# Kernel optimization log

Measured on AMD Instinct MI355X. Metric: run time of the kernel, lower is better.

## Reference

```python
import jax, jax.numpy as jnp
import numpy as np

# dims matching init_kwargs
B, C, T = 64, 8, 2048
K, DIL = 16, 4            # kernel_size, dilation
MLP = 16                  # mlp_dim
NF = min(MLP, K // 2 + 1) # n_frequencies = 9
FEAT = C * NF * 2         # 144
H1, H2 = 64, 32           # ReLUBlock hidden dims (64 -> 64//2)
EFF = DIL * (K - 1)       # 60
W = T - EFF               # 1988 windows


def setup_inputs() -> dict:
    key = jax.random.key(0)
    ks = jax.random.split(key, 10)
    def lin(k, out_d, in_d):
        kw, kb = jax.random.split(k)
        bound = 1.0 / np.sqrt(in_d)
        w = jax.random.uniform(kw, (out_d, in_d), jnp.float32, -bound, bound)
        b = jax.random.uniform(kb, (out_d,), jnp.float32, -bound, bound)
        return w, b
    x = jax.random.normal(ks[0], (B, C, T), jnp.float32)
    proj_w, proj_b = lin(ks[1], MLP, FEAT)
    w1, b1 = lin(ks[2], H1, MLP)
    w2, b2 = lin(ks[3], H2, H1)
    out_w, out_b = lin(ks[4], 1, H2)
    agg_w = jax.random.normal(ks[5], (W,), jnp.float32) * 0.1
    return {"x": x, "proj_w": proj_w, "proj_b": proj_b, "w1": w1, "b1": b1,
            "w2": w2, "b2": b2, "out_w": out_w, "out_b": out_b, "agg_w": agg_w}


def reference(x, proj_w, proj_b, w1, b1, w2, b2, out_w, out_b, agg_w):
    # Build all dilated windows at once: window[t, j] = x[..., t - (K-1-j)*DIL]
    starts = jnp.arange(EFF, T)                      # [W]
    offs = -(K - 1 - jnp.arange(K)) * DIL            # [K]
    idx = starts[:, None] + offs[None, :]            # [W, K]
    win = x[:, :, idx]                               # [B, C, W, K]
    f = jnp.fft.rfft(win, axis=-1)[..., :NF]         # [B, C, W, NF]
    mag = jnp.log1p(jnp.abs(f))
    ph = jnp.angle(f) / jnp.pi
    feat = jnp.stack([mag, ph], axis=-1)             # [B, C, W, NF, 2]
    feat = feat.transpose(0, 2, 1, 3, 4).reshape(B, W, FEAT)  # [B, W, C*NF*2]
    p = jnp.tanh(feat @ proj_w.T + proj_b) * jnp.pi  # [B, W, MLP]
    h = jax.nn.relu(p @ w1.T + b1)                   # [B, W, H1]
    h = jax.nn.relu(h @ w2.T + b2)                   # [B, W, H2]
    out = (h @ out_w.T + out_b)[..., 0]              # [B, W]
    wts = jax.nn.softmax(agg_w)                      # [W]
    return (out * wts[None, :]).sum(axis=1)          # [B]
```

## Files before the change

kernel.cpp:

```cpp
#include <hip/hip_runtime.h>
#include <math.h>

#define B_    64
#define C_    8
#define T_    2048
#define K_    16
#define NF_   9
#define FEAT_ 144
#define MLP_  16
#define H1_   64
#define H2_   32
#define EFF_  60
#define W_    1988
#define NWCH_ 8
#define PI_F  3.14159265358979323846f

constexpr float COS16[16] = {
   1.0f,  0.92387953251128674f,  0.70710678118654752f,  0.38268343236508977f,
   0.0f, -0.38268343236508977f, -0.70710678118654752f, -0.92387953251128674f,
  -1.0f, -0.92387953251128674f, -0.70710678118654752f, -0.38268343236508977f,
   0.0f,  0.38268343236508977f,  0.70710678118654752f,  0.92387953251128674f };
constexpr float SIN16[16] = {
   0.0f,  0.38268343236508977f,  0.70710678118654752f,  0.92387953251128674f,
   1.0f,  0.92387953251128674f,  0.70710678118654752f,  0.38268343236508977f,
   0.0f, -0.38268343236508977f, -0.70710678118654752f, -0.92387953251128674f,
   0.0f, -0.92387953251128674f, -0.70710678118654752f, -0.38268343236508977f };
constexpr float SIN16F[16] = {
   0.0f,  0.38268343236508977f,  0.70710678118654752f,  0.92387953251128674f,
   1.0f,  0.92387953251128674f,  0.70710678118654752f,  0.38268343236508977f,
   0.0f, -0.38268343236508977f, -0.70710678118654752f, -0.92387953251128674f,
  -1.0f, -0.92387953251128674f, -0.70710678118654752f, -0.38268343236508977f };

__device__ __forceinline__ float fast_log1p(float s) {
  return __builtin_amdgcn_logf(1.0f + s) * 0.69314718055994531f;
}

__device__ __forceinline__ float atanpi_poly(float r) {
  const float s2 = r * r;
  float p = -0.0037310f;
  p = fmaf(p, s2,  0.0167600f);
  p = fmaf(p, s2, -0.0370617f);
  p = fmaf(p, s2,  0.0616068f);
  p = fmaf(p, s2, -0.10587734f);
  p = fmaf(p, s2,  0.31830265f);
  return r * p;
}

__device__ __forceinline__ float atan2pi_fast(float im, float re) {
  const float ax = fabsf(re), ay = fabsf(im);
  const float mx = fmaxf(ax, ay), mn = fminf(ax, ay);
  const float r = mn * __builtin_amdgcn_rcpf(fmaxf(mx, 1e-37f));
  float t = atanpi_poly(r);
  t = (ay > ax) ? 0.5f - t : t;
  t = (__float_as_uint(re) & 0x80000000u) ? 1.0f - t : t;
  return copysignf(t, im);
}

__device__ __forceinline__ float fast_tanh(float z) {
  const float az = fabsf(z);
  const float e = __builtin_amdgcn_exp2f(-2.8853900817779268f * az);
  const float th = fmaf(-2.0f, e * __builtin_amdgcn_rcpf(1.0f + e), 1.0f);
  return copysignf(th, z);
}

__global__ __launch_bounds__(256) void prep_kernel(const float* __restrict__ pw,
                                                   const float* __restrict__ w2,
                                                   float* __restrict__ PWt,
                                                   float* __restrict__ W2t) {
  const int tid = blockIdx.x * 256 + threadIdx.x;
  if (tid < MLP_ * FEAT_) {
    const int j = tid / FEAT_, f = tid - j * FEAT_;
    PWt[f * MLP_ + j] = pw[tid];
  }
  if (tid < H2_ * H1_) {
    const int m = tid >> 6, i = tid & 63;
    W2t[i * H2_ + m] = w2[tid];
  }
}

__global__ __launch_bounds__(256) void softmax_kernel(const float* __restrict__ agg,
                                                      float* __restrict__ wts) {
  __shared__ float red[256];
  const int tid = threadIdx.x;
  float m = -INFINITY;
  for (int i = tid; i < W_; i += 256) m = fmaxf(m, agg[i]);
  red[tid] = m; __syncthreads();
  for (int s = 128; s > 0; s >>= 1) { if (tid < s) red[tid] = fmaxf(red[tid], red[tid+s]); __syncthreads(); }
  const float mx = red[0];
  __syncthreads();
  float sum = 0.f;
  for (int i = tid; i < W_; i += 256) sum += expf(agg[i] - mx);
  red[tid] = sum; __syncthreads();
  for (int s = 128; s > 0; s >>= 1) { if (tid < s) red[tid] += red[tid+s]; __syncthreads(); }
  const float inv = 1.f / red[0];
  for (int i = tid; i < W_; i += 256) wts[i] = expf(agg[i] - mx) * inv;
}

__global__ __launch_bounds__(256) void tcn_main(
    const float* __restrict__ x,
    const float* __restrict__ PWt, const float* __restrict__ proj_b,
    const float* __restrict__ w1, const float* __restrict__ b1,
    const float* __restrict__ W2t, const float* __restrict__ b2,
    const float* __restrict__ out_w, const float* __restrict__ out_b,
    const float* __restrict__ wts, float* __restrict__ partials) {
  __shared__ float red[256];
  const int tid = threadIdx.x;
  const int b = blockIdx.y;
  const int w = blockIdx.x * 256 + tid;
  float val = 0.f;
  if (w < W_) {
    float pacc[MLP_];
    #pragma unroll
    for (int j = 0; j < MLP_; j++) pacc[j] = proj_b[j];

    const float* xb = x + (size_t)(b * C_) * T_ + w;
    #pragma unroll 1
    for (int c = 0; c < C_; c++) {
      const float* xc = xb + c * T_;
      float win[K_];
      #pragma unroll
      for (int k = 0; k < K_; k++) win[k] = xc[k * 4];

      float ae[8], bo[8];
      #pragma unroll
      for (int k = 0; k < 8; k++) { ae[k] = win[k] + win[k+8]; bo[k] = win[k] - win[k+8]; }

      #pragma unroll
      for (int n = 0; n < NF_; n++) {
        float re = 0.f, im = 0.f;
        #pragma unroll
        for (int k = 0; k < 8; k++) {
          const float v = (n & 1) ? bo[k] : ae[k];
          const int t = (n * k) & 15;
          re = fmaf(v,  COS16[t],  re);
          im = fmaf(v, -SIN16F[t], im);
        }
        const float m2  = fmaf(re, re, im * im);
        const float s   = __builtin_amdgcn_sqrtf(m2);
        const float mag = fast_log1p(s);
        const float ph  = atan2pi_fast(im, re);

        const float* rm = PWt + (size_t)((c * NF_ + n) * 2) * MLP_;
        #pragma unroll
        for (int j = 0; j < MLP_; j++)
          pacc[j] = fmaf(mag, rm[j], fmaf(ph, rm[MLP_ + j], pacc[j]));
      }
    }

    float p[MLP_];
    #pragma unroll
    for (int j = 0; j < MLP_; j++) p[j] = fast_tanh(pacc[j]) * PI_F;

    float h2a[H2_];
    #pragma unroll
    for (int m = 0; m < H2_; m++) h2a[m] = b2[m];

    #pragma unroll 8
    for (int i = 0; i < H1_; i++) {
      const float* r1 = w1 + i * MLP_;
      float acc = b1[i];
      #pragma unroll
      for (int j = 0; j < MLP_; j++) acc = fmaf(p[j], r1[j], acc);
      const float h1v = fmaxf(acc, 0.f);
      const float* r2 = W2t + i * H2_;
      #pragma unroll
      for (int m = 0; m < H2_; m++) h2a[m] = fmaf(h1v, r2[m], h2a[m]);
    }

    float o = out_b[0];
    #pragma unroll
    for (int m = 0; m < H2_; m++) o = fmaf(fmaxf(h2a[m], 0.f), out_w[m], o);
    val = o * wts[w];
  }

  red[tid] = val; __syncthreads();
  for (int s = 128; s > 0; s >>= 1) { if (tid < s) red[tid] += red[tid+s]; __syncthreads(); }
  if (tid == 0) partials[b * gridDim.x + blockIdx.x] = red[0];
}

__global__ void finalize_kernel(const float* __restrict__ partials, float* __restrict__ out) {
  const int b = threadIdx.x;
  if (b < B_) {
    float s = 0.f;
    #pragma unroll
    for (int c = 0; c < NWCH_; c++) s += partials[b * NWCH_ + c];
    out[b] = s;
  }
}

extern "C" void kernel_launch(void* const* d_in, const int* in_sizes, int n_in,
                              void* d_out, int out_size, void* d_ws, size_t ws_size,
                              hipStream_t stream) {
  const float* x      = (const float*)d_in[0];
  const float* proj_w = (const float*)d_in[1];
  const float* proj_b = (const float*)d_in[2];
  const float* w1     = (const float*)d_in[3];
  const float* b1     = (const float*)d_in[4];
  const float* w2     = (const float*)d_in[5];
  const float* b2     = (const float*)d_in[6];
  const float* out_w  = (const float*)d_in[7];
  const float* out_b  = (const float*)d_in[8];
  const float* agg_w  = (const float*)d_in[9];

  float* wts      = (float*)d_ws;
  float* partials = (float*)d_ws + 2048;
  float* PWt      = (float*)d_ws + 4096;
  float* W2t      = (float*)d_ws + 4096 + 2304;

  prep_kernel<<<9, 256, 0, stream>>>(proj_w, w2, PWt, W2t);
  softmax_kernel<<<1, 256, 0, stream>>>(agg_w, wts);
  tcn_main<<<dim3(NWCH_, B_), 256, 0, stream>>>(x, PWt, proj_b, w1, b1, W2t, b2,
                                                out_w, out_b, wts, partials);
  finalize_kernel<<<1, 64, 0, stream>>>(partials, (float*)d_out);
}
```

Measured before the change: 60.71 us.

## Split each window across four waves over channels and hidden units

Each block now handles 64 windows instead of 256. Its four waves split the per-window work: each wave computes the DFT features for two channels and 16 of the 64 first-hidden units. Partial projection sums and partial second-layer sums are combined through shared memory, and the final reduction uses wave shuffles. The grid grows from 512 to 2048 blocks so more waves can run on the GPU at once. In exchange it adds several block barriers and shared-memory traffic, and the finalize kernel sums 32 partials per batch row.

```diff
diff --git a/kernel.cpp b/kernel.cpp
--- a/kernel.cpp
+++ b/kernel.cpp
@@ -12,7 +12,7 @@
 #define H2_   32
 #define EFF_  60
 #define W_    1988
-#define NWCH_ 8
+#define NCHK_ 32
 #define PI_F  3.14159265358979323846f
 
 constexpr float COS16[16] = {
@@ -20,11 +20,6 @@
    0.0f, -0.38268343236508977f, -0.70710678118654752f, -0.92387953251128674f,
   -1.0f, -0.92387953251128674f, -0.70710678118654752f, -0.38268343236508977f,
    0.0f,  0.38268343236508977f,  0.70710678118654752f,  0.92387953251128674f };
-constexpr float SIN16[16] = {
-   0.0f,  0.38268343236508977f,  0.70710678118654752f,  0.92387953251128674f,
-   1.0f,  0.92387953251128674f,  0.70710678118654752f,  0.38268343236508977f,
-   0.0f, -0.38268343236508977f, -0.70710678118654752f, -0.92387953251128674f,
-   0.0f, -0.92387953251128674f, -0.70710678118654752f, -0.38268343236508977f };
 constexpr float SIN16F[16] = {
    0.0f,  0.38268343236508977f,  0.70710678118654752f,  0.92387953251128674f,
    1.0f,  0.92387953251128674f,  0.70710678118654752f,  0.38268343236508977f,
@@ -103,79 +98,110 @@
     const float* __restrict__ W2t, const float* __restrict__ b2,
     const float* __restrict__ out_w, const float* __restrict__ out_b,
     const float* __restrict__ wts, float* __restrict__ partials) {
-  __shared__ float red[256];
-  const int tid = threadIdx.x;
-  const int b = blockIdx.y;
-  const int w = blockIdx.x * 256 + tid;
-  float val = 0.f;
-  if (w < W_) {
-    float pacc[MLP_];
-    #pragma unroll
-    for (int j = 0; j < MLP_; j++) pacc[j] = proj_b[j];
-
-    const float* xb = x + (size_t)(b * C_) * T_ + w;
-    #pragma unroll 1
-    for (int c = 0; c < C_; c++) {
-      const float* xc = xb + c * T_;
-      float win[K_];
+  __shared__ float buf[4096];
+  const int tid  = threadIdx.x;
+  const int lane = tid & 63;
+  const int cg   = tid >> 6;
+  const int b     = blockIdx.y;
+  const int chunk = blockIdx.x;
+  const int w  = chunk * 64 + lane;
+  const int wl = (w < W_) ? w : (W_ - 1);
+
+  float pacc[MLP_];
+  #pragma unroll
+  for (int j = 0; j < MLP_; j++) pacc[j] = 0.f;
+
+  #pragma unroll
+  for (int cc = 0; cc < 2; cc++) {
+    const int c = cg + cc * 4;
+    const float* xc = x + ((size_t)b * C_ + c) * T_ + wl;
+    float win[K_];
+    #pragma unroll
+    for (int k = 0; k < K_; k++) win[k] = xc[k * 4];
+
+    float ae[8], bo[8];
+    #pragma unroll
+    for (int k = 0; k < 8; k++) { ae[k] = win[k] + win[k+8]; bo[k] = win[k] - win[k+8]; }
+
+    #pragma unroll
+    for (int n = 0; n < NF_; n++) {
+      float re = 0.f, im = 0.f;
       #pragma unroll
-      for (int k = 0; k < K_; k++) win[k] = xc[k * 4];
-
-      float ae[8], bo[8];
+      for (int k = 0; k < 8; k++) {
+        const float v = (n & 1) ? bo[k] : ae[k];
+        const int t = (n * k) & 15;
+        re = fmaf(v,  COS16[t],  re);
+        im = fmaf(v, -SIN16F[t], im);
+      }
+      const float s   = __builtin_amdgcn_sqrtf(fmaf(re, re, im * im));
+      const float mag = fast_log1p(s);
+      const float ph  = atan2pi_fast(im, re);
+      const float* rm = PWt + (size_t)((c * NF_ + n) * 2) * MLP_;
       #pragma unroll
-      for (int k = 0; k < 8; k++) { ae[k] = win[k] + win[k+8]; bo[k] = win[k] - win[k+8]; }
-
-      #pragma unroll
-      for (int n = 0; n < NF_; n++) {
-        float re = 0.f, im = 0.f;
-        #pragma unroll
-        for (int k = 0; k < 8; k++) {
-          const float v = (n & 1) ? bo[k] : ae[k];
-          const int t = (n * k) & 15;
-          re = fmaf(v,  COS16[t],  re);
-          im = fmaf(v, -SIN16F[t], im);
-        }
-        const float m2  = fmaf(re, re, im * im);
-        const float s   = __builtin_amdgcn_sqrtf(m2);
-        const float mag = fast_log1p(s);
-        const float ph  = atan2pi_fast(im, re);
-
-        const float* rm = PWt + (size_t)((c * NF_ + n) * 2) * MLP_;
-        #pragma unroll
-        for (int j = 0; j < MLP_; j++)
-          pacc[j] = fmaf(mag, rm[j], fmaf(ph, rm[MLP_ + j], pacc[j]));
-      }
+      for (int j = 0; j < MLP_; j++)
+        pacc[j] = fmaf(mag, rm[j], fmaf(ph, rm[MLP_ + j], pacc[j]));
     }
-
-    float p[MLP_];
-    #pragma unroll
-    for (int j = 0; j < MLP_; j++) p[j] = fast_tanh(pacc[j]) * PI_F;
-
-    float h2a[H2_];
-    #pragma unroll
-    for (int m = 0; m < H2_; m++) h2a[m] = b2[m];
-
-    #pragma unroll 8
-    for (int i = 0; i < H1_; i++) {
-      const float* r1 = w1 + i * MLP_;
-      float acc = b1[i];
-      #pragma unroll
-      for (int j = 0; j < MLP_; j++) acc = fmaf(p[j], r1[j], acc);
-      const float h1v = fmaxf(acc, 0.f);
-      const float* r2 = W2t + i * H2_;
-      #pragma unroll
-      for (int m = 0; m < H2_; m++) h2a[m] = fmaf(h1v, r2[m], h2a[m]);
+  }
+
+  #pragma unroll
+  for (int j = 0; j < MLP_; j++) buf[(j * 4 + cg) * 64 + lane] = pacc[j];
+  __syncthreads();
+
+  float p[MLP_];
+  #pragma unroll
+  for (int j = 0; j < MLP_; j++) {
+    const float* r = &buf[j * 256];
+    const float s01 = r[lane] + r[64 + lane];
+    const float s23 = r[128 + lane] + r[192 + lane];
+    p[j] = fast_tanh(s01 + s23 + proj_b[j]) * PI_F;
+  }
+  __syncthreads();
+
+  float h2a[H2_];
+  #pragma unroll
+  for (int m = 0; m < H2_; m++) h2a[m] = 0.f;
+
+  #pragma unroll 4
+  for (int ii = 0; ii < 16; ii++) {
+    const int i = cg * 16 + ii;
+    const float* r1 = w1 + i * MLP_;
+    float acc = b1[i];
+    #pragma unroll
+    for (int j = 0; j < MLP_; j++) acc = fmaf(p[j], r1[j], acc);
+    const float h1v = fmaxf(acc, 0.f);
+    const float* r2 = W2t + i * H2_;
+    #pragma unroll
+    for (int m = 0; m < H2_; m++) h2a[m] = fmaf(h1v, r2[m], h2a[m]);
+  }
+
+  if (cg >= 2) {
+    #pragma unroll
+    for (int m = 0; m < H2_; m++) buf[(m * 2 + (cg - 2)) * 64 + lane] = h2a[m];
+  }
+  __syncthreads();
+  if (cg < 2) {
+    #pragma unroll
+    for (int m = 0; m < H2_; m++) h2a[m] += buf[(m * 2 + cg) * 64 + lane];
+  }
+  __syncthreads();
+  if (cg == 1) {
+    #pragma unroll
+    for (int m = 0; m < H2_; m++) buf[(m * 2) * 64 + lane] = h2a[m];
+  }
+  __syncthreads();
+
+  if (cg == 0) {
+    float o = out_b[0];
+    #pragma unroll
+    for (int m = 0; m < H2_; m++) {
+      const float h2v = h2a[m] + buf[(m * 2) * 64 + lane] + b2[m];
+      o = fmaf(fmaxf(h2v, 0.f), out_w[m], o);
     }
-
-    float o = out_b[0];
-    #pragma unroll
-    for (int m = 0; m < H2_; m++) o = fmaf(fmaxf(h2a[m], 0.f), out_w[m], o);
-    val = o * wts[w];
-  }
-
-  red[tid] = val; __syncthreads();
-  for (int s = 128; s > 0; s >>= 1) { if (tid < s) red[tid] += red[tid+s]; __syncthreads(); }
-  if (tid == 0) partials[b * gridDim.x + blockIdx.x] = red[0];
+    float val = (w < W_) ? o * wts[wl] : 0.f;
+    #pragma unroll
+    for (int s = 32; s >= 1; s >>= 1) val += __shfl_xor(val, s, 64);
+    if (lane == 0) partials[b * NCHK_ + chunk] = val;
+  }
 }
 
 __global__ void finalize_kernel(const float* __restrict__ partials, float* __restrict__ out) {
@@ -183,7 +209,7 @@
   if (b < B_) {
     float s = 0.f;
     #pragma unroll
-    for (int c = 0; c < NWCH_; c++) s += partials[b * NWCH_ + c];
+    for (int c = 0; c < NCHK_; c++) s += partials[b * NCHK_ + c];
     out[b] = s;
   }
 }
@@ -209,7 +235,7 @@
 
   prep_kernel<<<9, 256, 0, stream>>>(proj_w, w2, PWt, W2t);
   softmax_kernel<<<1, 256, 0, stream>>>(agg_w, wts);
-  tcn_main<<<dim3(NWCH_, B_), 256, 0, stream>>>(x, PWt, proj_b, w1, b1, W2t, b2,
+  tcn_main<<<dim3(NCHK_, B_), 256, 0, stream>>>(x, PWt, proj_b, w1, b1, W2t, b2,
                                                 out_w, out_b, wts, partials);
   finalize_kernel<<<1, 64, 0, stream>>>(partials, (float*)d_out);
 }
```

Measured after the change: 98.30 us. 61.9% more time.

## Split DFT projection across channel groups into separate stage with workspace partials

Applied to the files above, without the earlier changes.

Splits the main kernel into two stages. Stage 1 computes the DFT features and projection partial sums for pairs of channels across four times as many blocks, raising parallelism beyond the original 512 blocks, and writes 16-float partials to workspace. Stage 2 sums the partials, then runs the tanh and MLP tail and the weighted reduction. The softmax and weight-transpose prep are merged into one setup kernel to save a launch. This adds an intermediate write and read of about 32 MB plus one extra launch, and falls back to the monolithic kernel if the workspace is too small.

```diff
diff --git a/kernel.cpp b/kernel.cpp
--- a/kernel.cpp
+++ b/kernel.cpp
@@ -13,6 +13,7 @@
 #define EFF_  60
 #define W_    1988
 #define NWCH_ 8
+#define NG_   4
 #define PI_F  3.14159265358979323846f
 
 constexpr float COS16[16] = {
@@ -20,11 +21,6 @@
    0.0f, -0.38268343236508977f, -0.70710678118654752f, -0.92387953251128674f,
   -1.0f, -0.92387953251128674f, -0.70710678118654752f, -0.38268343236508977f,
    0.0f,  0.38268343236508977f,  0.70710678118654752f,  0.92387953251128674f };
-constexpr float SIN16[16] = {
-   0.0f,  0.38268343236508977f,  0.70710678118654752f,  0.92387953251128674f,
-   1.0f,  0.92387953251128674f,  0.70710678118654752f,  0.38268343236508977f,
-   0.0f, -0.38268343236508977f, -0.70710678118654752f, -0.92387953251128674f,
-   0.0f, -0.92387953251128674f, -0.70710678118654752f, -0.38268343236508977f };
 constexpr float SIN16F[16] = {
    0.0f,  0.38268343236508977f,  0.70710678118654752f,  0.92387953251128674f,
    1.0f,  0.92387953251128674f,  0.70710678118654752f,  0.38268343236508977f,
@@ -63,46 +59,120 @@
   return copysignf(th, z);
 }
 
-__global__ __launch_bounds__(256) void prep_kernel(const float* __restrict__ pw,
-                                                   const float* __restrict__ w2,
-                                                   float* __restrict__ PWt,
-                                                   float* __restrict__ W2t) {
-  const int tid = blockIdx.x * 256 + threadIdx.x;
-  if (tid < MLP_ * FEAT_) {
-    const int j = tid / FEAT_, f = tid - j * FEAT_;
-    PWt[f * MLP_ + j] = pw[tid];
-  }
-  if (tid < H2_ * H1_) {
-    const int m = tid >> 6, i = tid & 63;
-    W2t[i * H2_ + m] = w2[tid];
-  }
-}
-
-__global__ __launch_bounds__(256) void softmax_kernel(const float* __restrict__ agg,
-                                                      float* __restrict__ wts) {
-  __shared__ float red[256];
+__device__ __forceinline__ void dft_proj_channel(const float* __restrict__ xc,
+                                                 const float* __restrict__ PWt,
+                                                 int c, float* pacc) {
+  float win[K_];
+  #pragma unroll
+  for (int k = 0; k < K_; k++) win[k] = xc[k * 4];
+  float ae[8], bo[8];
+  #pragma unroll
+  for (int k = 0; k < 8; k++) { ae[k] = win[k] + win[k+8]; bo[k] = win[k] - win[k+8]; }
+  #pragma unroll
+  for (int n = 0; n < NF_; n++) {
+    float re = 0.f, im = 0.f;
+    #pragma unroll
+    for (int k = 0; k < 8; k++) {
+      const float v = (n & 1) ? bo[k] : ae[k];
+      const int t = (n * k) & 15;
+      re = fmaf(v,  COS16[t],  re);
+      im = fmaf(v, -SIN16F[t], im);
+    }
+    const float s   = __builtin_amdgcn_sqrtf(fmaf(re, re, im * im));
+    const float mag = fast_log1p(s);
+    const float ph  = atan2pi_fast(im, re);
+    const float* rm = PWt + (size_t)((c * NF_ + n) * 2) * MLP_;
+    #pragma unroll
+    for (int j = 0; j < MLP_; j++)
+      pacc[j] = fmaf(mag, rm[j], fmaf(ph, rm[MLP_ + j], pacc[j]));
+  }
+}
+
+__device__ __forceinline__ float mlp_tail(const float* p,
+                                          const float* __restrict__ w1, const float* __restrict__ b1,
+                                          const float* __restrict__ W2t, const float* __restrict__ b2,
+                                          const float* __restrict__ out_w, const float* __restrict__ out_b) {
+  float h2a[H2_];
+  #pragma unroll
+  for (int m = 0; m < H2_; m++) h2a[m] = b2[m];
+  #pragma unroll 8
+  for (int i = 0; i < H1_; i++) {
+    const float* r1 = w1 + i * MLP_;
+    float acc = b1[i];
+    #pragma unroll
+    for (int j = 0; j < MLP_; j++) acc = fmaf(p[j], r1[j], acc);
+    const float h1v = fmaxf(acc, 0.f);
+    const float* r2 = W2t + i * H2_;
+    #pragma unroll
+    for (int m = 0; m < H2_; m++) h2a[m] = fmaf(h1v, r2[m], h2a[m]);
+  }
+  float o = out_b[0];
+  #pragma unroll
+  for (int m = 0; m < H2_; m++) o = fmaf(fmaxf(h2a[m], 0.f), out_w[m], o);
+  return o;
+}
+
+__global__ __launch_bounds__(256) void setup_kernel(const float* __restrict__ agg,
+                                                    float* __restrict__ wts,
+                                                    const float* __restrict__ pw,
+                                                    const float* __restrict__ w2,
+                                                    float* __restrict__ PWt,
+                                                    float* __restrict__ W2t) {
+  if (blockIdx.x == 0) {
+    __shared__ float red[256];
+    const int tid = threadIdx.x;
+    float m = -INFINITY;
+    for (int i = tid; i < W_; i += 256) m = fmaxf(m, agg[i]);
+    red[tid] = m; __syncthreads();
+    for (int s = 128; s > 0; s >>= 1) { if (tid < s) red[tid] = fmaxf(red[tid], red[tid+s]); __syncthreads(); }
+    const float mx = red[0];
+    __syncthreads();
+    float sum = 0.f;
+    for (int i = tid; i < W_; i += 256) sum += expf(agg[i] - mx);
+    red[tid] = sum; __syncthreads();
+    for (int s = 128; s > 0; s >>= 1) { if (tid < s) red[tid] += red[tid+s]; __syncthreads(); }
+    const float inv = 1.f / red[0];
+    for (int i = tid; i < W_; i += 256) wts[i] = expf(agg[i] - mx) * inv;
+  } else {
+    const int tid = (blockIdx.x - 1) * 256 + threadIdx.x;
+    if (tid < MLP_ * FEAT_) {
+      const int j = tid / FEAT_, f = tid - j * FEAT_;
+      PWt[f * MLP_ + j] = pw[tid];
+    }
+    if (tid < H2_ * H1_) {
+      const int m = tid >> 6, i = tid & 63;
+      W2t[i * H2_ + m] = w2[tid];
+    }
+  }
+}
+
+__global__ __launch_bounds__(256) void tcn_stage1(const float* __restrict__ x,
+                                                  const float* __restrict__ PWt,
+                                                  float* __restrict__ pf) {
   const int tid = threadIdx.x;
-  float m = -INFINITY;
-  for (int i = tid; i < W_; i += 256) m = fmaxf(m, agg[i]);
-  red[tid] = m; __syncthreads();
-  for (int s = 128; s > 0; s >>= 1) { if (tid < s) red[tid] = fmaxf(red[tid], red[tid+s]); __syncthreads(); }
-  const float mx = red[0];
-  __syncthreads();
-  float sum = 0.f;
-  for (int i = tid; i < W_; i += 256) sum += expf(agg[i] - mx);
-  red[tid] = sum; __syncthreads();
-  for (int s = 128; s > 0; s >>= 1) { if (tid < s) red[tid] += red[tid+s]; __syncthreads(); }
-  const float inv = 1.f / red[0];
-  for (int i = tid; i < W_; i += 256) wts[i] = expf(agg[i] - mx) * inv;
-}
-
-__global__ __launch_bounds__(256) void tcn_main(
-    const float* __restrict__ x,
-    const float* __restrict__ PWt, const float* __restrict__ proj_b,
-    const float* __restrict__ w1, const float* __restrict__ b1,
-    const float* __restrict__ W2t, const float* __restrict__ b2,
-    const float* __restrict__ out_w, const float* __restrict__ out_b,
-    const float* __restrict__ wts, float* __restrict__ partials) {
+  const int b = blockIdx.y, g = blockIdx.z;
+  const int w = blockIdx.x * 256 + tid;
+  if (w >= W_) return;
+  float pacc[MLP_];
+  #pragma unroll
+  for (int j = 0; j < MLP_; j++) pacc[j] = 0.f;
+  #pragma unroll 1
+  for (int cc = 0; cc < 2; cc++) {
+    const int c = g * 2 + cc;
+    dft_proj_channel(x + ((size_t)b * C_ + c) * T_ + w, PWt, c, pacc);
+  }
+  float4* dst = reinterpret_cast<float4*>(pf + ((size_t)(b * NG_ + g) * W_ + w) * MLP_);
+  #pragma unroll
+  for (int q = 0; q < 4; q++)
+    dst[q] = make_float4(pacc[4*q+0], pacc[4*q+1], pacc[4*q+2], pacc[4*q+3]);
+}
+
+__global__ __launch_bounds__(256) void tcn_stage2(const float* __restrict__ pf,
+                                                  const float* __restrict__ proj_b,
+                                                  const float* __restrict__ w1, const float* __restrict__ b1,
+                                                  const float* __restrict__ W2t, const float* __restrict__ b2,
+                                                  const float* __restrict__ out_w, const float* __restrict__ out_b,
+                                                  const float* __restrict__ wts, float* __restrict__ partials) {
   __shared__ float red[256];
   const int tid = threadIdx.x;
   const int b = blockIdx.y;
@@ -112,70 +182,51 @@
     float pacc[MLP_];
     #pragma unroll
     for (int j = 0; j < MLP_; j++) pacc[j] = proj_b[j];
-
-    const float* xb = x + (size_t)(b * C_) * T_ + w;
-    #pragma unroll 1
-    for (int c = 0; c < C_; c++) {
-      const float* xc = xb + c * T_;
-      float win[K_];
+    #pragma unroll
+    for (int g = 0; g < NG_; g++) {
+      const float4* src = reinterpret_cast<const float4*>(pf + ((size_t)(b * NG_ + g) * W_ + w) * MLP_);
       #pragma unroll
-      for (int k = 0; k < K_; k++) win[k] = xc[k * 4];
-
-      float ae[8], bo[8];
-      #pragma unroll
-      for (int k = 0; k < 8; k++) { ae[k] = win[k] + win[k+8]; bo[k] = win[k] - win[k+8]; }
-
-      #pragma unroll
-      for (int n = 0; n < NF_; n++) {
-        float re = 0.f, im = 0.f;
-        #pragma unroll
-        for (int k = 0; k < 8; k++) {
-          const float v = (n & 1) ? bo[k] : ae[k];
-          const int t = (n * k) & 15;
-          re = fmaf(v,  COS16[t],  re);
-          im = fmaf(v, -SIN16F[t], im);
-        }
-        const float m2  = fmaf(re, re, im * im);
-        const float s   = __builtin_amdgcn_sqrtf(m2);
-        const float mag = fast_log1p(s);
-        const float ph  = atan2pi_fast(im, re);
-
-        const float* rm = PWt + (size_t)((c * NF_ + n) * 2) * MLP_;
-        #pragma unroll
-        for (int j = 0; j < MLP_; j++)
-          pacc[j] = fmaf(mag, rm[j], fmaf(ph, rm[MLP_ + j], pacc[j]));
+      for (int q = 0; q < 4; q++) {
+        const float4 a = src[q];
+        pacc[4*q+0] += a.x; pacc[4*q+1] += a.y; pacc[4*q+2] += a.z; pacc[4*q+3] += a.w;
       }
     }
-
     float p[MLP_];
     #pragma unroll
     for (int j = 0; j < MLP_; j++) p[j] = fast_tanh(pacc[j]) * PI_F;
-
-    float h2a[H2_];
-    #pragma unroll
-    for (int m = 0; m < H2_; m++) h2a[m] = b2[m];
-
-    #pragma unroll 8
-    for (int i = 0; i < H1_; i++) {
-      const float* r1 = w1 + i * MLP_;
-      float acc = b1[i];
-      #pragma unroll
-      for (int j = 0; j < MLP_; j++) acc = fmaf(p[j], r1[j], acc);
-      const float h1v = fmaxf(acc, 0.f);
-      const float* r2 = W2t + i * H2_;
-      #pragma unroll
-      for (int m = 0; m < H2_; m++) h2a[m] = fmaf(h1v, r2[m], h2a[m]);
-    }
-
-    float o = out_b[0];
-    #pragma unroll
-    for (int m = 0; m < H2_; m++) o = fmaf(fmaxf(h2a[m], 0.f), out_w[m], o);
-    val = o * wts[w];
-  }
-
+    val = mlp_tail(p, w1, b1, W2t, b2, out_w, out_b) * wts[w];
+  }
   red[tid] = val; __syncthreads();
   for (int s = 128; s > 0; s >>= 1) { if (tid < s) red[tid] += red[tid+s]; __syncthreads(); }
-  if (tid == 0) partials[b * gridDim.x + blockIdx.x] = red[0];
+  if (tid == 0) partials[b * NWCH_ + blockIdx.x] = red[0];
+}
+
+__global__ __launch_bounds__(256) void tcn_mono(const float* __restrict__ x,
+                                                const float* __restrict__ PWt, const float* __restrict__ proj_b,
+                                                const float* __restrict__ w1, const float* __restrict__ b1,
+                                                const float* __restrict__ W2t, const float* __restrict__ b2,
+                                                const float* __restrict__ out_w, const float* __restrict__ out_b,
+                                                const float* __restrict__ wts, float* __restrict__ partials) {
+  __shared__ float red[256];
+  const int tid = threadIdx.x;
+  const int b = blockIdx.y;
+  const int w = blockIdx.x * 256 + tid;
+  float val = 0.f;
+  if (w < W_) {
+    float pacc[MLP_];
+    #pragma unroll
+    for (int j = 0; j < MLP_; j++) pacc[j] = proj_b[j];
+    #pragma unroll 1
+    for (int c = 0; c < C_; c++)
+      dft_proj_channel(x + ((size_t)b * C_ + c) * T_ + w, PWt, c, pacc);
+    float p[MLP_];
+    #pragma unroll
+    for (int j = 0; j < MLP_; j++) p[j] = fast_tanh(pacc[j]) * PI_F;
+    val = mlp_tail(p, w1, b1, W2t, b2, out_w, out_b) * wts[w];
+  }
+  red[tid] = val; __syncthreads();
+  for (int s = 128; s > 0; s >>= 1) { if (tid < s) red[tid] += red[tid+s]; __syncthreads(); }
+  if (tid == 0) partials[b * NWCH_ + blockIdx.x] = red[0];
 }
 
 __global__ void finalize_kernel(const float* __restrict__ partials, float* __restrict__ out) {
@@ -206,10 +257,18 @@
   float* partials = (float*)d_ws + 2048;
   float* PWt      = (float*)d_ws + 4096;
   float* W2t      = (float*)d_ws + 4096 + 2304;
-
-  prep_kernel<<<9, 256, 0, stream>>>(proj_w, w2, PWt, W2t);
-  softmax_kernel<<<1, 256, 0, stream>>>(agg_w, wts);
-  tcn_main<<<dim3(NWCH_, B_), 256, 0, stream>>>(x, PWt, proj_b, w1, b1, W2t, b2,
-                                                out_w, out_b, wts, partials);
+  float* pf       = (float*)d_ws + 16384;
+
+  const size_t need = ((size_t)16384 + (size_t)B_ * NG_ * W_ * MLP_) * sizeof(float);
+
+  setup_kernel<<<10, 256, 0, stream>>>(agg_w, wts, proj_w, w2, PWt, W2t);
+  if (ws_size >= need) {
+    tcn_stage1<<<dim3(NWCH_, B_, NG_), 256, 0, stream>>>(x, PWt, pf);
+    tcn_stage2<<<dim3(NWCH_, B_), 256, 0, stream>>>(pf, proj_b, w1, b1, W2t, b2,
+                                                    out_w, out_b, wts, partials);
+  } else {
+    tcn_mono<<<dim3(NWCH_, B_), 256, 0, stream>>>(x, PWt, proj_b, w1, b1, W2t, b2,
+                                                  out_w, out_b, wts, partials);
+  }
   finalize_kernel<<<1, 64, 0, stream>>>(partials, (float*)d_out);
 }
```

After: 64.85 us. 1.07x slower.
